# Kernel optimization log

Hardware: AMD Instinct MI355X
Metric: run time of the kernel (lower is better)

The kernel has to match this reference:

```python
import jax, jax.numpy as jnp
from jax import lax
import numpy as np

# inferred ssconv semantics (custom CUDA kernel not in source):
#  - input x: (B, H, W, Cin) channels-last, Cin = per-pixel channel count
#  - in_index: (B, H, W) in [0, IN_GROUPS): routes each input pixel's Cin channels
#    to the corresponding slice of the weight's input-channel dim (gather/scatter MoE-style dispatch)
#  - weight: (OUT_GROUPS*Cout, IN_GROUPS*Cin, kh, kw), bias: (OUT_GROUPS*Cout,)
#  - per output pixel, one out-group is selected (maxout over groups); the kernel
#    returns both the selected Cout channels and the winning group index (out_index)

IN_GROUPS = 4
OUT_GROUPS = 4
STRIDE = 1  # pad = stride//2 in the wrapper; output (H-1)//s+1 == SAME padding


def setup_inputs() -> dict:
    key = jax.random.key(0)
    k1, k2, k3, k4 = jax.random.split(key, 4)
    x = jax.random.normal(k1, (8, 256, 256, 16), dtype=jnp.float32)
    in_index = jax.random.randint(k2, (8, 256, 256), 0, IN_GROUPS, dtype=jnp.int32)
    weight = jax.random.normal(k3, (64, 64, 3, 3), dtype=jnp.float32) * 0.05
    bias = jax.random.normal(k4, (64,), dtype=jnp.float32) * 0.05
    return {"x": x, "in_index": in_index, "weight": weight, "bias": bias}


def reference(x, in_index, weight, bias):
    B, H, W, Cin = x.shape
    OC, IC, kh, kw = weight.shape  # OC = OUT_GROUPS*Cout, IC = IN_GROUPS*Cin
    Cout = OC // OUT_GROUPS

    # dispatch: scatter each pixel's channels into its in-group slice (rest zero)
    onehot = jax.nn.one_hot(in_index, IN_GROUPS, dtype=x.dtype)          # (B,H,W,G)
    x_full = (onehot[..., :, None] * x[..., None, :]).reshape(B, H, W, IN_GROUPS * Cin)

    # dense conv over the dispatched tensor == per-pixel gathered group weights
    w_hwio = jnp.transpose(weight, (2, 3, 1, 0))  # (kh,kw,IC,OC)
    out = lax.conv_general_dilated(
        x_full, w_hwio, window_strides=(STRIDE, STRIDE), padding="SAME",
        dimension_numbers=("NHWC", "HWIO", "NHWC"))
    out = out + bias  # (B,H',W',OC)

    Bo, Ho, Wo, _ = out.shape
    out_g = out.reshape(Bo, Ho, Wo, OUT_GROUPS, Cout)
    scores = out_g.max(axis=-1)                    # (B,H',W',G) per-group response
    out_index = jnp.argmax(scores, axis=-1)        # winning out-group per pixel
    sel = jnp.take_along_axis(out_g, out_index[..., None, None], axis=3)
    sel = jnp.squeeze(sel, axis=3)                 # (B,H',W',Cout)
    return sel, out_index.astype(jnp.int32)
```

## Files before the change

kernel.cpp:

```cpp
#include <hip/hip_runtime.h>

#define H 256
#define W 256
#define BATCH 8
#define CIN 16
#define TW 64
#define TH 8
#define HWC (TW + 2)
#define HHC (TH + 2)
#define NHALO (HWC * HHC)
#define FIX_CAP 16384
#define GAP_TAU 2e-3f

#define OFF_XH   73728
#define OFF_XL   84288
#define OFF_GS   94848
#define OFF_SW   97488
#define OFF_BIAS 97744
#define OFF_RED  98000
#define SMEM_BYTES 98032

typedef __attribute__((ext_vector_type(4))) int i32x4;

__device__ __forceinline__ void gload_lds16(const void* g, void* l) {
    __builtin_amdgcn_global_load_lds(
        (const __attribute__((address_space(1))) unsigned int*)g,
        (__attribute__((address_space(3))) unsigned int*)l, 16, 0, 0);
}

__device__ __forceinline__ float4 add4(float4 a, float4 b) {
    return make_float4(a.x + b.x, a.y + b.y, a.z + b.z, a.w + b.w);
}
__device__ __forceinline__ float max4(float4 a) {
    return fmaxf(fmaxf(a.x, a.y), fmaxf(a.z, a.w));
}

__global__ void wprep_kernel(const float* __restrict__ w, char* __restrict__ wt,
                             float* __restrict__ sw_ws, unsigned* __restrict__ fix_cnt) {
    const int n = blockIdx.x;
    const int k = threadIdx.x;
    if (n == 0 && k == 0) fix_cnt[0] = 0u;

    float v[9];
    float m = 0.f;
#pragma unroll
    for (int t = 0; t < 9; ++t) {
        v[t] = w[(n * 64 + k) * 9 + t];
        m = fmaxf(m, fabsf(v[t]));
    }
#pragma unroll
    for (int s = 1; s < 64; s <<= 1) m = fmaxf(m, __shfl_xor(m, s, 64));
    const float inv = (m > 0.f) ? (127.f / m) : 0.f;
    if (k == 0) sw_ws[n] = m * (1.f / 127.f);

    const int nt = n >> 4, nl = n & 15, kq = k >> 4, j = k & 15;
    const int lane16 = (kq * 16 + nl) * 16 + j;
#pragma unroll
    for (int t = 0; t < 9; ++t) {
        float f = v[t] * inv;
        int h = __float2int_rn(f);
        int l = __float2int_rn((f - (float)h) * 128.f);
        wt[((t * 2 + 0) * 4 + nt) * 1024 + lane16] = (char)h;
        wt[((t * 2 + 1) * 4 + nt) * 1024 + lane16] = (char)l;
    }
}

__global__ __launch_bounds__(512, 2) void ssconv_i8_kernel(
    const float* __restrict__ x, const int* __restrict__ gidx,
    const char* __restrict__ wt, const float* __restrict__ sw_ws,
    const float* __restrict__ bias,
    float* __restrict__ out_sel, float* __restrict__ out_idx,
    unsigned* __restrict__ fix_cnt, unsigned* __restrict__ fix_list)
{
    __shared__ __align__(16) char smem[SMEM_BYTES];
    char*  bufB  = smem;
    char*  xhL   = smem + OFF_XH;
    char*  xlL   = smem + OFF_XL;
    int*   gsL   = (int*)(smem + OFF_GS);
    float* swdL  = (float*)(smem + OFF_SW);
    float* biasL = (float*)(smem + OFF_BIAS);
    float* redL  = (float*)(smem + OFF_RED);
    float* outS  = (float*)smem;

    const int tid  = threadIdx.x;
    const int x0   = blockIdx.x * TW;
    const int y0   = blockIdx.y * TH;
    const int bz   = blockIdx.z;
    const int wvid = tid >> 6;
    const int L    = tid & 63;
    const int q    = L >> 4;
    const int lm   = L & 15;

#pragma unroll
    for (int it = 0; it < 9; ++it)
        gload_lds16(wt + it * 8192 + tid * 16, bufB + it * 8192 + tid * 16);

    if (tid < 64) { swdL[tid] = sw_ws[tid]; biasL[tid] = bias[tid]; }

    float4 av[2][4];
    int gv[2];
    float am = 0.f;
#pragma unroll
    for (int s = 0; s < 2; ++s) {
        av[s][0] = av[s][1] = av[s][2] = av[s][3] = make_float4(0, 0, 0, 0);
        gv[s] = 0;
        int i = tid + s * 512;
        if (i < NHALO) {
            int r = i / HWC, c = i - r * HWC;
            int hy = y0 + r - 1, hx = x0 + c - 1;
            if (hy >= 0 && hy < H && hx >= 0 && hx < W) {
                const float4* src = (const float4*)(x + (((size_t)bz * H + hy) * W + hx) * CIN);
                av[s][0] = src[0]; av[s][1] = src[1]; av[s][2] = src[2]; av[s][3] = src[3];
                gv[s] = gidx[((size_t)bz * H + hy) * W + hx];
            }
#pragma unroll
            for (int j = 0; j < 4; ++j)
                am = fmaxf(am, fmaxf(fmaxf(fabsf(av[s][j].x), fabsf(av[s][j].y)),
                                     fmaxf(fabsf(av[s][j].z), fabsf(av[s][j].w))));
        }
    }
#pragma unroll
    for (int s = 1; s < 64; s <<= 1) am = fmaxf(am, __shfl_xor(am, s, 64));
    if (L == 0) redL[wvid] = am;
    __syncthreads();
    float bm = redL[0];
#pragma unroll
    for (int wv = 1; wv < 8; ++wv) bm = fmaxf(bm, redL[wv]);
    const float qinv = (bm > 0.f) ? (127.f / bm) : 0.f;
    const float sB   = bm * (1.f / 127.f);

#pragma unroll
    for (int s = 0; s < 2; ++s) {
        int i = tid + s * 512;
        if (i < NHALO) {
            unsigned hw[4], lw[4];
#pragma unroll
            for (int j = 0; j < 4; ++j) {
                float fs[4] = {av[s][j].x, av[s][j].y, av[s][j].z, av[s][j].w};
                unsigned hword = 0, lword = 0;
#pragma unroll
                for (int e = 0; e < 4; ++e) {
                    float f_ = fs[e] * qinv;
                    int h_ = __float2int_rn(f_);
                    int l_ = __float2int_rn((f_ - (float)h_) * 128.f);
                    hword |= ((unsigned)(h_ & 255)) << (8 * e);
                    lword |= ((unsigned)(l_ & 255)) << (8 * e);
                }
                hw[j] = hword; lw[j] = lword;
            }
            *(uint4*)&xhL[(size_t)i * 16] = make_uint4(hw[0], hw[1], hw[2], hw[3]);
            *(uint4*)&xlL[(size_t)i * 16] = make_uint4(lw[0], lw[1], lw[2], lw[3]);
            gsL[i] = gv[s];
        }
    }
    __syncthreads();

    i32x4 acc1[4][4] = {};
    i32x4 acc2[4][4] = {};

#pragma unroll 1
    for (int tap = 0; tap < 9; ++tap) {
        const int dy = tap / 3, dx = tap - dy * 3;
        const int hbase = (wvid + dy) * HWC + lm + dx;
        const char* bB = bufB + tap * 8192;

        i32x4 bh[4], bl[4];
#pragma unroll
        for (int nt = 0; nt < 4; ++nt) {
            bh[nt] = *(const i32x4*)(bB + nt * 1024 + L * 16);
            bl[nt] = *(const i32x4*)(bB + 4096 + nt * 1024 + L * 16);
        }
#pragma unroll
        for (int m = 0; m < 4; ++m) {
            int hb = hbase + 16 * m;
            int gg = gsL[hb];
            i32x4 ah = *(const i32x4*)&xhL[(size_t)hb * 16];
            i32x4 al = *(const i32x4*)&xlL[(size_t)hb * 16];
            bool keep = (gg == q);
            i32x4 z = {};
            i32x4 a0 = keep ? ah : z;
            i32x4 a1 = keep ? al : z;
#pragma unroll
            for (int nt = 0; nt < 4; ++nt) {
                acc1[m][nt] = __builtin_amdgcn_mfma_i32_16x16x64_i8(a0, bh[nt], acc1[m][nt], 0, 0, 0);
                acc2[m][nt] = __builtin_amdgcn_mfma_i32_16x16x64_i8(a0, bl[nt], acc2[m][nt], 0, 0, 0);
                acc2[m][nt] = __builtin_amdgcn_mfma_i32_16x16x64_i8(a1, bh[nt], acc2[m][nt], 0, 0, 0);
            }
        }
    }
    __syncthreads();

    float swb[4];
#pragma unroll
    for (int nt = 0; nt < 4; ++nt) swb[nt] = sB * swdL[nt * 16 + lm];

#pragma unroll
    for (int pass = 0; pass < 2; ++pass) {
#pragma unroll
        for (int mh = 0; mh < 2; ++mh) {
            const int m = pass * 2 + mh;
            const int prow = wvid * 32 + mh * 16 + q * 4;
#pragma unroll
            for (int nt = 0; nt < 4; ++nt)
#pragma unroll
                for (int r = 0; r < 4; ++r) {
                    float v = swb[nt] *
                              ((float)acc1[m][nt][r] + (float)acc2[m][nt][r] * (1.f / 128.f));
                    outS[(prow + r) * 68 + nt * 16 + lm] = v;
                }
        }
        __syncthreads();

        {
            int p  = tid >> 1;
            int hh = tid & 1;
            const float4* srcp = (const float4*)(outS + p * 68 + hh * 32);
            const float4* bb2  = (const float4*)(biasL + hh * 32);
            float4 r0 = add4(srcp[0], bb2[0]), r1 = add4(srcp[1], bb2[1]);
            float4 r2 = add4(srcp[2], bb2[2]), r3 = add4(srcp[3], bb2[3]);
            float4 r4 = add4(srcp[4], bb2[4]), r5 = add4(srcp[5], bb2[5]);
            float4 r6 = add4(srcp[6], bb2[6]), r7 = add4(srcp[7], bb2[7]);

            float ma = fmaxf(fmaxf(max4(r0), max4(r1)), fmaxf(max4(r2), max4(r3)));
            float mb = fmaxf(fmaxf(max4(r4), max4(r5)), fmaxf(max4(r6), max4(r7)));
            float pa = __shfl_xor(ma, 1, 64);
            float pb = __shfl_xor(mb, 1, 64);
            float s0, s1, s2, s3;
            if (hh == 0) { s0 = ma; s1 = mb; s2 = pa; s3 = pb; }
            else         { s0 = pa; s1 = pb; s2 = ma; s3 = mb; }
            int bg = 0; float best = s0;
            if (s1 > best) { best = s1; bg = 1; }
            if (s2 > best) { best = s2; bg = 2; }
            if (s3 > best) { best = s3; bg = 3; }

            int wv = p >> 5;
            int gy = y0 + wv, gx = x0 + pass * 32 + (p & 31);
            size_t opix = ((size_t)bz * H + gy) * W + gx;
            if ((bg >> 1) == hh) {
                bool useB = (bg & 1) != 0;
                float4 o0 = useB ? r4 : r0, o1 = useB ? r5 : r1;
                float4 o2 = useB ? r6 : r2, o3 = useB ? r7 : r3;
                float4* os = (float4*)(out_sel + opix * 16);
                os[0] = o0; os[1] = o1; os[2] = o2; os[3] = o3;
            }
            if (hh == 0) {
                out_idx[opix] = (float)bg;
                float o1v = (bg == 0) ? s1 : s0;
                float o2v = (bg <= 1) ? s2 : s1;
                float o3v = (bg <= 2) ? s3 : s2;
                float second = fmaxf(o1v, fmaxf(o2v, o3v));
                if (best - second < GAP_TAU) {
                    unsigned slot = atomicAdd(fix_cnt, 1u);
                    if (slot < FIX_CAP) fix_list[slot] = (unsigned)opix;
                }
            }
        }
        __syncthreads();
    }
}

__global__ void fixup_kernel(const float* __restrict__ x, const int* __restrict__ gidx,
                             const float* __restrict__ w, const float* __restrict__ bias,
                             float* __restrict__ out_sel, float* __restrict__ out_idx,
                             const unsigned* __restrict__ fix_cnt,
                             const unsigned* __restrict__ fix_list)
{
    unsigned n = *fix_cnt;
    if (n > FIX_CAP) n = FIX_CAP;
    const int lane = threadIdx.x & 63;
    const int nwaves = gridDim.x * (blockDim.x >> 6);
    unsigned widx = blockIdx.x * (blockDim.x >> 6) + (threadIdx.x >> 6);

    for (; widx < n; widx += nwaves) {
        unsigned opix = fix_list[widx];
        int b  = opix >> 16;
        int y  = (opix >> 8) & 255;
        int xc = opix & 255;
        double acc = (double)bias[lane];
        for (int dy = 0; dy < 3; ++dy) {
            int yy = y + dy - 1;
            if (yy < 0 || yy >= H) continue;
            for (int dx = 0; dx < 3; ++dx) {
                int xx = xc + dx - 1;
                if (xx < 0 || xx >= W) continue;
                size_t pix = ((size_t)b * H + yy) * W + xx;
                int g = gidx[pix];
                const float* xp = x + pix * 16;
                const float* wp = w + (size_t)(lane * 64 + g * 16) * 9 + (dy * 3 + dx);
#pragma unroll
                for (int c = 0; c < 16; ++c)
                    acc = fma((double)wp[c * 9], (double)xp[c], acc);
            }
        }
        double m = acc;
        m = fmax(m, __shfl_xor(m, 1, 64));
        m = fmax(m, __shfl_xor(m, 2, 64));
        m = fmax(m, __shfl_xor(m, 4, 64));
        m = fmax(m, __shfl_xor(m, 8, 64));
        double g0 = __shfl(m, 0, 64), g1 = __shfl(m, 16, 64);
        double g2 = __shfl(m, 32, 64), g3 = __shfl(m, 48, 64);
        int bg = 0; double bb = g0;
        if (g1 > bb) { bb = g1; bg = 1; }
        if (g2 > bb) { bb = g2; bg = 2; }
        if (g3 > bb) { bb = g3; bg = 3; }
        if ((lane >> 4) == bg) out_sel[(size_t)opix * 16 + (lane & 15)] = (float)acc;
        if (lane == 0) out_idx[opix] = (float)bg;
    }
}

extern "C" void kernel_launch(void* const* d_in, const int* in_sizes, int n_in,
                              void* d_out, int out_size, void* d_ws, size_t ws_size,
                              hipStream_t stream) {
    const float* x    = (const float*)d_in[0];
    const int*   gidx = (const int*)d_in[1];
    const float* w    = (const float*)d_in[2];
    const float* bias = (const float*)d_in[3];

    char*     wt       = (char*)d_ws;
    float*    sw_ws    = (float*)((char*)d_ws + 73728);
    unsigned* fix_cnt  = (unsigned*)((char*)d_ws + 73984);
    unsigned* fix_list = (unsigned*)((char*)d_ws + 74000);

    float* out_sel = (float*)d_out;
    float* out_idx = (float*)d_out + (size_t)BATCH * H * W * CIN;

    wprep_kernel<<<64, 64, 0, stream>>>(w, wt, sw_ws, fix_cnt);

    dim3 grid(W / TW, H / TH, BATCH);
    ssconv_i8_kernel<<<grid, 512, 0, stream>>>(x, gidx, wt, sw_ws, bias,
                                               out_sel, out_idx, fix_cnt, fix_list);
    fixup_kernel<<<256, 256, 0, stream>>>(x, gidx, w, bias, out_sel, out_idx,
                                          fix_cnt, fix_list);
}
```

Before: 227.3 us.

## Double-buffer per-tap weights and do argmax in registers to shrink LDS

Instead of staging all nine taps of quantized weights in LDS up front, the kernel now double-buffers one tap at a time, prefetching the next tap while computing the current one with a barrier per tap. The epilogue no longer stages results through LDS; it applies scale and bias in registers and computes per-group maxima with cross-lane shuffles, then writes each selected channel directly. LDS use drops from about 96KB to about 40KB and launch bounds rise to 4 blocks per CU to raise occupancy. The costs are nine barriers in the main loop, possible exposure of weight-load latency, more shuffle work, and scalar rather than float4 output stores.

```diff
diff --git a/kernel.cpp b/kernel.cpp
--- a/kernel.cpp
+++ b/kernel.cpp
@@ -12,13 +12,13 @@
 #define FIX_CAP 16384
 #define GAP_TAU 2e-3f
 
-#define OFF_XH   73728
-#define OFF_XL   84288
-#define OFF_GS   94848
-#define OFF_SW   97488
-#define OFF_BIAS 97744
-#define OFF_RED  98000
-#define SMEM_BYTES 98032
+#define OFF_XH   16384
+#define OFF_XL   26944
+#define OFF_GS   37504
+#define OFF_SW   40144
+#define OFF_BIAS 40400
+#define OFF_RED  40656
+#define SMEM_BYTES 40688
 
 typedef __attribute__((ext_vector_type(4))) int i32x4;
 
@@ -26,13 +26,6 @@
     __builtin_amdgcn_global_load_lds(
         (const __attribute__((address_space(1))) unsigned int*)g,
         (__attribute__((address_space(3))) unsigned int*)l, 16, 0, 0);
-}
-
-__device__ __forceinline__ float4 add4(float4 a, float4 b) {
-    return make_float4(a.x + b.x, a.y + b.y, a.z + b.z, a.w + b.w);
-}
-__device__ __forceinline__ float max4(float4 a) {
-    return fmaxf(fmaxf(a.x, a.y), fmaxf(a.z, a.w));
 }
 
 __global__ void wprep_kernel(const float* __restrict__ w, char* __restrict__ wt,
@@ -65,7 +58,7 @@
     }
 }
 
-__global__ __launch_bounds__(512, 2) void ssconv_i8_kernel(
+__global__ __launch_bounds__(512, 4) void ssconv_i8_kernel(
     const float* __restrict__ x, const int* __restrict__ gidx,
     const char* __restrict__ wt, const float* __restrict__ sw_ws,
     const float* __restrict__ bias,
@@ -80,7 +73,6 @@
     float* swdL  = (float*)(smem + OFF_SW);
     float* biasL = (float*)(smem + OFF_BIAS);
     float* redL  = (float*)(smem + OFF_RED);
-    float* outS  = (float*)smem;
 
     const int tid  = threadIdx.x;
     const int x0   = blockIdx.x * TW;
@@ -91,9 +83,7 @@
     const int q    = L >> 4;
     const int lm   = L & 15;
 
-#pragma unroll
-    for (int it = 0; it < 9; ++it)
-        gload_lds16(wt + it * 8192 + tid * 16, bufB + it * 8192 + tid * 16);
+    gload_lds16(wt + tid * 16, bufB + tid * 16);
 
     if (tid < 64) { swdL[tid] = sw_ws[tid]; biasL[tid] = bias[tid]; }
 
@@ -160,9 +150,13 @@
 
 #pragma unroll 1
     for (int tap = 0; tap < 9; ++tap) {
+        if (tap < 8)
+            gload_lds16(wt + (size_t)(tap + 1) * 8192 + tid * 16,
+                        bufB + ((tap + 1) & 1) * 8192 + tid * 16);
+
+        const char* bB = bufB + (tap & 1) * 8192;
         const int dy = tap / 3, dx = tap - dy * 3;
         const int hbase = (wvid + dy) * HWC + lm + dx;
-        const char* bB = bufB + tap * 8192;
 
         i32x4 bh[4], bl[4];
 #pragma unroll
@@ -187,67 +181,50 @@
                 acc2[m][nt] = __builtin_amdgcn_mfma_i32_16x16x64_i8(a1, bh[nt], acc2[m][nt], 0, 0, 0);
             }
         }
-    }
-    __syncthreads();
-
-    float swb[4];
-#pragma unroll
-    for (int nt = 0; nt < 4; ++nt) swb[nt] = sB * swdL[nt * 16 + lm];
-
-#pragma unroll
-    for (int pass = 0; pass < 2; ++pass) {
-#pragma unroll
-        for (int mh = 0; mh < 2; ++mh) {
-            const int m = pass * 2 + mh;
-            const int prow = wvid * 32 + mh * 16 + q * 4;
-#pragma unroll
-            for (int nt = 0; nt < 4; ++nt)
-#pragma unroll
-                for (int r = 0; r < 4; ++r) {
-                    float v = swb[nt] *
-                              ((float)acc1[m][nt][r] + (float)acc2[m][nt][r] * (1.f / 128.f));
-                    outS[(prow + r) * 68 + nt * 16 + lm] = v;
-                }
-        }
         __syncthreads();
-
-        {
-            int p  = tid >> 1;
-            int hh = tid & 1;
-            const float4* srcp = (const float4*)(outS + p * 68 + hh * 32);
-            const float4* bb2  = (const float4*)(biasL + hh * 32);
-            float4 r0 = add4(srcp[0], bb2[0]), r1 = add4(srcp[1], bb2[1]);
-            float4 r2 = add4(srcp[2], bb2[2]), r3 = add4(srcp[3], bb2[3]);
-            float4 r4 = add4(srcp[4], bb2[4]), r5 = add4(srcp[5], bb2[5]);
-            float4 r6 = add4(srcp[6], bb2[6]), r7 = add4(srcp[7], bb2[7]);
-
-            float ma = fmaxf(fmaxf(max4(r0), max4(r1)), fmaxf(max4(r2), max4(r3)));
-            float mb = fmaxf(fmaxf(max4(r4), max4(r5)), fmaxf(max4(r6), max4(r7)));
-            float pa = __shfl_xor(ma, 1, 64);
-            float pb = __shfl_xor(mb, 1, 64);
-            float s0, s1, s2, s3;
-            if (hh == 0) { s0 = ma; s1 = mb; s2 = pa; s3 = pb; }
-            else         { s0 = pa; s1 = pb; s2 = ma; s3 = mb; }
-            int bg = 0; float best = s0;
-            if (s1 > best) { best = s1; bg = 1; }
-            if (s2 > best) { best = s2; bg = 2; }
-            if (s3 > best) { best = s3; bg = 3; }
-
-            int wv = p >> 5;
-            int gy = y0 + wv, gx = x0 + pass * 32 + (p & 31);
-            size_t opix = ((size_t)bz * H + gy) * W + gx;
-            if ((bg >> 1) == hh) {
-                bool useB = (bg & 1) != 0;
-                float4 o0 = useB ? r4 : r0, o1 = useB ? r5 : r1;
-                float4 o2 = useB ? r6 : r2, o3 = useB ? r7 : r3;
-                float4* os = (float4*)(out_sel + opix * 16);
-                os[0] = o0; os[1] = o1; os[2] = o2; os[3] = o3;
-            }
-            if (hh == 0) {
+    }
+
+    float swb[4], bsr[4];
+#pragma unroll
+    for (int nt = 0; nt < 4; ++nt) {
+        swb[nt] = sB * swdL[nt * 16 + lm];
+        bsr[nt] = biasL[nt * 16 + lm];
+    }
+
+    const int gy = y0 + wvid;
+#pragma unroll
+    for (int m = 0; m < 4; ++m) {
+#pragma unroll
+        for (int r = 0; r < 4; ++r) {
+            float v0 = swb[0] * ((float)acc1[m][0][r] + (float)acc2[m][0][r] * (1.f / 128.f)) + bsr[0];
+            float v1 = swb[1] * ((float)acc1[m][1][r] + (float)acc2[m][1][r] * (1.f / 128.f)) + bsr[1];
+            float v2 = swb[2] * ((float)acc1[m][2][r] + (float)acc2[m][2][r] * (1.f / 128.f)) + bsr[2];
+            float v3 = swb[3] * ((float)acc1[m][3][r] + (float)acc2[m][3][r] * (1.f / 128.f)) + bsr[3];
+
+            float g0 = v0, g1 = v1, g2 = v2, g3 = v3;
+#pragma unroll
+            for (int s = 1; s < 16; s <<= 1) {
+                g0 = fmaxf(g0, __shfl_xor(g0, s, 64));
+                g1 = fmaxf(g1, __shfl_xor(g1, s, 64));
+                g2 = fmaxf(g2, __shfl_xor(g2, s, 64));
+                g3 = fmaxf(g3, __shfl_xor(g3, s, 64));
+            }
+            int bg = 0; float best = g0;
+            if (g1 > best) { best = g1; bg = 1; }
+            if (g2 > best) { best = g2; bg = 2; }
+            if (g3 > best) { best = g3; bg = 3; }
+
+            float selv = (bg == 0) ? v0 : (bg == 1) ? v1 : (bg == 2) ? v2 : v3;
+
+            const int gx = x0 + m * 16 + q * 4 + r;
+            const size_t opix = ((size_t)bz * H + gy) * W + gx;
+            out_sel[opix * 16 + lm] = selv;
+
+            if (lm == 0) {
                 out_idx[opix] = (float)bg;
-                float o1v = (bg == 0) ? s1 : s0;
-                float o2v = (bg <= 1) ? s2 : s1;
-                float o3v = (bg <= 2) ? s3 : s2;
+                float o1v = (bg == 0) ? g1 : g0;
+                float o2v = (bg <= 1) ? g2 : g1;
+                float o3v = (bg <= 2) ? g3 : g2;
                 float second = fmaxf(o1v, fmaxf(o2v, o3v));
                 if (best - second < GAP_TAU) {
                     unsigned slot = atomicAdd(fix_cnt, 1u);
@@ -255,7 +232,6 @@
                 }
             }
         }
-        __syncthreads();
     }
 }
 
```

Result: slower. 573.8 us (+152.5%).
